# Performance work log

Measured on AMD Instinct MI355X. Metric: run time of the kernel, lower is better.

Reference implementation:

```python
import jax, jax.numpy as jnp
import numpy as np

WS = (4, 4, 4)          # window size (D, H, W)
DIM = 96
HEADS = 8
HEAD_DIM = DIM // HEADS
SCALE = HEAD_DIM ** (-0.5)
N = WS[0] * WS[1] * WS[2]  # 64 tokens per window


def _relative_position_index(ws):
    coords = np.stack(np.meshgrid(np.arange(ws[0]), np.arange(ws[1]), np.arange(ws[2]), indexing='ij'))
    cf = coords.reshape(3, -1)                       # [3, N]
    rel = cf[:, :, None] - cf[:, None, :]            # [3, N, N]
    rel = rel.transpose(1, 2, 0).astype(np.int64)    # [N, N, 3]
    rel[:, :, 0] += ws[0] - 1
    rel[:, :, 1] += ws[1] - 1
    rel[:, :, 2] += ws[2] - 1
    rel[:, :, 0] *= (2 * ws[1] - 1) * (2 * ws[2] - 1)
    rel[:, :, 1] *= 2 * ws[2] - 1
    return jnp.asarray(rel.sum(-1))                  # [N, N]

REL_IDX = _relative_position_index(WS)


def setup_inputs() -> dict:
    key = jax.random.key(0)
    ks = jax.random.split(key, 6)
    B = 4096   # total windows (64 images x 64 windows)
    nW = 64
    table_size = (2 * WS[0] - 1) * (2 * WS[1] - 1) * (2 * WS[2] - 1)  # 343
    return {
        'x': jax.random.normal(ks[0], (B, N, DIM), jnp.float32),
        'mask': jax.random.normal(ks[1], (nW, N, N), jnp.float32),
        'qkv_w': jax.random.normal(ks[2], (3 * DIM, DIM), jnp.float32) * 0.02,
        'proj_w': jax.random.normal(ks[3], (DIM, DIM), jnp.float32) * 0.02,
        'proj_b': jnp.zeros((DIM,), jnp.float32),
        'bias_table': jax.random.normal(ks[4], (table_size, HEADS), jnp.float32) * 0.02,
    }


def reference(x, mask, qkv_w, proj_w, proj_b, bias_table):
    B, n, C = x.shape
    # QKV projection (torch Linear: y = x @ W.T), split into heads
    qkv = (x @ qkv_w.T).reshape(B, n, 3, HEADS, HEAD_DIM)
    qkv = jnp.transpose(qkv, (2, 0, 3, 1, 4))        # [3, B, H, N, hd]
    q, k, v = qkv[0], qkv[1], qkv[2]
    attn = jnp.einsum('bhnd,bhmd->bhnm', q, k) * SCALE
    # gathered relative position bias: [N, N, H] -> [H, N, N]
    bias = bias_table[REL_IDX[:n, :n].reshape(-1)].reshape(n, n, HEADS)
    attn = attn + jnp.transpose(bias, (2, 0, 1))[None]
    # shifted-window mask add
    nW = mask.shape[0]
    attn = attn.reshape(B // nW, nW, HEADS, n, n) + mask[None, :, None]
    attn = attn.reshape(B, HEADS, n, n)
    attn = jax.nn.softmax(attn, axis=-1)
    out = jnp.einsum('bhnm,bhmd->bnhd', attn, v).reshape(B, n, C)
    return out @ proj_w.T + proj_b
```

## Files before the change

### kernel.cpp

```cpp
#include <hip/hip_runtime.h>
#include <hip/hip_bf16.h>
#include <stdint.h>


typedef float  f32x4  __attribute__((ext_vector_type(4)));
typedef float  f32x16 __attribute__((ext_vector_type(16)));
typedef short  short8 __attribute__((ext_vector_type(8)));

#define WS_WQKV_OFF  (8388608)
#define WS_WPROJ_OFF (8388608 + 55296)
#define LOG2E 1.4426950408889634f

__device__ __forceinline__ unsigned short f2bf(float f) {
  __hip_bfloat16 h = __float2bfloat16(f);
  return *reinterpret_cast<unsigned short*>(&h);
}
__device__ __forceinline__ uint32_t pack2(float a, float b) {
  __hip_bfloat162 h = __float22bfloat162_rn(float2{a, b});
  return *reinterpret_cast<uint32_t*>(&h);
}

__global__ void prep_weights(const float* __restrict__ qkv_w,
                             const float* __restrict__ proj_w,
                             unsigned short* __restrict__ ws16) {
  int tid = blockIdx.x * 256 + threadIdx.x;
  if (tid < 27648) {
    float v = qkv_w[tid];
    if (tid < 9216) v *= (0.28867513459481288f * LOG2E);
    ws16[WS_WQKV_OFF / 2 + tid] = f2bf(v);
  } else {
    int t = tid - 27648;
    ws16[WS_WPROJ_OFF / 2 + t] = f2bf(proj_w[t]);
  }
}

__global__ void prep_biasm(const float* __restrict__ mask,
                           const float* __restrict__ bias_table,
                           float* __restrict__ biasm) {
  int tid = blockIdx.x * 256 + threadIdx.x;
  int m = tid & 63;
  int r = (tid >> 6) & 63;
  int h = (tid >> 12) & 7;
  int w = tid >> 15;
  int dr = r >> 4, hr = (r >> 2) & 3, wr = r & 3;
  int dm = m >> 4, hm = (m >> 2) & 3, wm = m & 3;
  int idx = (dr - dm + 3) * 49 + (hr - hm + 3) * 7 + (wr - wm + 3);
  biasm[tid] = (bias_table[idx * 8 + h] + mask[(w * 64 + r) * 64 + m]) * LOG2E;
}

__global__ __launch_bounds__(512, 4) void attn_main(
    const float* __restrict__ x, const float* __restrict__ proj_b,
    const unsigned short* __restrict__ ws16, const float* __restrict__ biasm,
    float* __restrict__ out) {
  __shared__ __align__(16) unsigned short xo[64][104];
  __shared__ __align__(16) unsigned short q_s[8][64][24];
  __shared__ __align__(16) unsigned short k_s[8][64][24];
  __shared__ __align__(16) unsigned short v_s[8][16][72];

  const int tid  = threadIdx.x;
  const int wv   = tid >> 6;
  const int lane = tid & 63;
  const int lo4 = lane & 15, hi4 = lane >> 4;
  const int lo5 = lane & 31, hi5 = lane >> 5;
  const int blk = blockIdx.x;
  const int wmask = blk & 63;

  const unsigned short* wqkv  = ws16 + WS_WQKV_OFF / 2;
  const unsigned short* wproj = ws16 + WS_WPROJ_OFF / 2;

  {
    int h = tid >> 6, r = tid & 63;
    *(uint2*)&q_s[h][r][12] = make_uint2(0u, 0u);
    *(uint2*)&k_s[h][r][12] = make_uint2(0u, 0u);
  }

  {
    const float4* xsrc = (const float4*)(x + (size_t)blk * (64 * 96));
    for (int i = tid; i < 1536; i += 512) {
      float4 v = xsrc[i];
      int t = i / 24, c4 = (i % 24) * 4;
      uint2 w2;
      w2.x = pack2(v.x, v.y);
      w2.y = pack2(v.z, v.w);
      *(uint2*)&xo[t][c4] = w2;
    }
  }
  __syncthreads();

  {
    const int sub = wv & 3;
    const int par = wv >> 2;
    const int trow = sub * 16 + lo4;
    f32x4 acc[9];
#pragma unroll
    for (int i = 0; i < 9; ++i) acc[i] = (f32x4){0.f, 0.f, 0.f, 0.f};
#pragma unroll
    for (int ks = 0; ks < 3; ++ks) {
      short8 bfX = *(const short8*)&xo[trow][ks * 32 + hi4 * 8];
#pragma unroll
      for (int i = 0; i < 9; ++i) {
        const int mt = 2 * i + par;
        short8 afW = *(const short8*)&wqkv[(mt * 16 + lo4) * 96 + ks * 32 + hi4 * 8];
        acc[i] = __builtin_amdgcn_mfma_f32_16x16x32_bf16(afW, bfX, acc[i], 0, 0, 0);
      }
    }
#pragma unroll
    for (int i = 0; i < 9; ++i) {
      const int mt = 2 * i + par;
      const int o0 = mt * 16 + hi4 * 4;
      if (o0 < 192) {
        const int sec = (o0 >= 96) ? 96 : 0;
        const int o = o0 - sec;
        const int head = o / 12, ch = o - head * 12;
        uint2 w2;
        w2.x = pack2(acc[i][0], acc[i][1]);
        w2.y = pack2(acc[i][2], acc[i][3]);
        if (sec == 0) *(uint2*)&q_s[head][trow][ch] = w2;
        else          *(uint2*)&k_s[head][trow][ch] = w2;
      } else {
        const int o = o0 - 192;
        const int head = o / 12, ch = o - head * 12;
#pragma unroll
        for (int j = 0; j < 4; ++j)
          v_s[head][ch + j][trow] = f2bf(acc[i][j]);
      }
    }
  }

  f32x16 c[2][2];
  {
    const float* bm = biasm + (size_t)(wmask * 8 + wv) * 4096;
#pragma unroll
    for (int ti = 0; ti < 2; ++ti)
#pragma unroll
      for (int tj = 0; tj < 2; ++tj)
#pragma unroll
        for (int q4 = 0; q4 < 4; ++q4) {
          float4 b4 = *(const float4*)&bm[(tj * 32 + lo5) * 64 + ti * 32 + 8 * q4 + 4 * hi5];
          c[ti][tj][4 * q4 + 0] = b4.x;
          c[ti][tj][4 * q4 + 1] = b4.y;
          c[ti][tj][4 * q4 + 2] = b4.z;
          c[ti][tj][4 * q4 + 3] = b4.w;
        }
  }
  __syncthreads();

  {
    const int h = wv;
#pragma unroll
    for (int ti = 0; ti < 2; ++ti) {
      short8 af = *(const short8*)&k_s[h][ti * 32 + lo5][hi5 * 8];
#pragma unroll
      for (int tj = 0; tj < 2; ++tj) {
        short8 bf = *(const short8*)&q_s[h][tj * 32 + lo5][hi5 * 8];
        c[ti][tj] = __builtin_amdgcn_mfma_f32_32x32x16_bf16(af, bf, c[ti][tj], 0, 0, 0);
      }
    }

#pragma unroll
    for (int tj = 0; tj < 2; ++tj) {
      float mx = -1e30f;
#pragma unroll
      for (int ti = 0; ti < 2; ++ti)
#pragma unroll
        for (int reg = 0; reg < 16; ++reg) mx = fmaxf(mx, c[ti][tj][reg]);
      mx = fmaxf(mx, __shfl_xor(mx, 32));
      float sum = 0.f;
#pragma unroll
      for (int ti = 0; ti < 2; ++ti)
#pragma unroll
        for (int reg = 0; reg < 16; ++reg) {
          float e = exp2f(c[ti][tj][reg] - mx);
          c[ti][tj][reg] = e;
          sum += e;
        }
      sum += __shfl_xor(sum, 32);
      float rs = 1.0f / sum;
#pragma unroll
      for (int ti = 0; ti < 2; ++ti)
#pragma unroll
        for (int reg = 0; reg < 16; ++reg) c[ti][tj][reg] *= rs;
    }

    uint32_t pkp[2][2][8];
#pragma unroll
    for (int ti = 0; ti < 2; ++ti)
#pragma unroll
      for (int tj = 0; tj < 2; ++tj)
#pragma unroll
        for (int u = 0; u < 8; ++u)
          pkp[ti][tj][u] = pack2(c[ti][tj][2 * u], c[ti][tj][2 * u + 1]);

    f32x16 oD[2];
    oD[0] = (f32x16)(0.f); oD[1] = (f32x16)(0.f);
#pragma unroll
    for (int kc = 0; kc < 4; ++kc) {
      const int ti = kc >> 1, base = 4 * (kc & 1);
      short8 av = *(const short8*)&v_s[h][lo5 & 15][kc * 16 + hi5 * 8];
#pragma unroll
      for (int tj = 0; tj < 2; ++tj) {
        uint32_t A0 = pkp[ti][tj][base + 0], A1 = pkp[ti][tj][base + 1];
        uint32_t A2 = pkp[ti][tj][base + 2], A3 = pkp[ti][tj][base + 3];
        uint32_t k0 = hi5 ? A2 : A0, k1 = hi5 ? A3 : A1;
        uint32_t s0 = (uint32_t)__shfl_xor((int)(hi5 ? A0 : A2), 32);
        uint32_t s1 = (uint32_t)__shfl_xor((int)(hi5 ? A1 : A3), 32);
        union { uint32_t u[4]; short8 s; } bfr;
        bfr.u[0] = hi5 ? s0 : k0;
        bfr.u[1] = hi5 ? s1 : k1;
        bfr.u[2] = hi5 ? k0 : s0;
        bfr.u[3] = hi5 ? k1 : s1;
        oD[tj] = __builtin_amdgcn_mfma_f32_32x32x16_bf16(av, bfr.s, oD[tj], 0, 0, 0);
      }
    }

#pragma unroll
    for (int tj = 0; tj < 2; ++tj) {
      const int q = tj * 32 + lo5;
      uint2 w2;
      w2.x = pack2(oD[tj][0], oD[tj][1]);
      w2.y = pack2(oD[tj][2], oD[tj][3]);
      *(uint2*)&xo[q][h * 12 + 4 * hi5] = w2;
      if (hi5 == 0) {
        uint2 w3;
        w3.x = pack2(oD[tj][4], oD[tj][5]);
        w3.y = pack2(oD[tj][6], oD[tj][7]);
        *(uint2*)&xo[q][h * 12 + 8] = w3;
      }
    }
  }
  __syncthreads();

  {
    const int mt = wv >> 1;
    const int nb = (wv & 1) * 3;
    f32x4 acc[3];
#pragma unroll
    for (int nt = 0; nt < 3; ++nt) acc[nt] = (f32x4){0.f, 0.f, 0.f, 0.f};
    const int arow = mt * 16 + lo4;
#pragma unroll
    for (int ks = 0; ks < 3; ++ks) {
      short8 af = *(const short8*)&xo[arow][ks * 32 + hi4 * 8];
#pragma unroll
      for (int nt = 0; nt < 3; ++nt) {
        const int ntg = nb + nt;
        short8 bf = *(const short8*)&wproj[(ntg * 16 + lo4) * 96 + ks * 32 + hi4 * 8];
        acc[nt] = __builtin_amdgcn_mfma_f32_16x16x32_bf16(af, bf, acc[nt], 0, 0, 0);
      }
    }
    float* od = out + (size_t)blk * (64 * 96);
#pragma unroll
    for (int nt = 0; nt < 3; ++nt) {
      const int ntg = nb + nt;
      float pb = proj_b[ntg * 16 + lo4];
#pragma unroll
      for (int j = 0; j < 4; ++j)
        od[(mt * 16 + hi4 * 4 + j) * 96 + ntg * 16 + lo4] = acc[nt][j] + pb;
    }
  }
}

extern "C" void kernel_launch(void* const* d_in, const int* in_sizes, int n_in,
                              void* d_out, int out_size, void* d_ws, size_t ws_size,
                              hipStream_t stream) {
  const float* x          = (const float*)d_in[0];
  const float* mask       = (const float*)d_in[1];
  const float* qkv_w      = (const float*)d_in[2];
  const float* proj_w     = (const float*)d_in[3];
  const float* proj_b     = (const float*)d_in[4];
  const float* bias_table = (const float*)d_in[5];

  float* biasm = (float*)d_ws;
  unsigned short* ws16 = (unsigned short*)d_ws;

  prep_weights<<<144, 256, 0, stream>>>(qkv_w, proj_w, ws16);
  prep_biasm<<<8192, 256, 0, stream>>>(mask, bias_table, biasm);
  attn_main<<<4096, 512, 0, stream>>>(x, proj_b, ws16, biasm, (float*)d_out);
}
```

Baseline: 180.6 us.

## Cut shared memory footprint: register-load x, shrink q/k padding, alias output on v_s

Drops the LDS staging buffer for x. Each wave now loads its own x rows straight from global memory into registers and converts them to bf16 fragments, which also removes one barrier. The q/k LDS rows shrink from 24 to 16 elements, and the attention output is written into an alias of the v_s buffer, which costs an extra barrier before it is overwritten. With LDS usage falling from about 81KB to about 51KB, more blocks can fit per CU, and launch bounds are raised from 4 to 6. The risks are register pressure or spills under the tighter bound and possible LDS bank conflicts from the smaller row stride.

```diff
diff --git a/kernel.cpp b/kernel.cpp
--- a/kernel.cpp
+++ b/kernel.cpp
@@ -48,13 +48,12 @@
   biasm[tid] = (bias_table[idx * 8 + h] + mask[(w * 64 + r) * 64 + m]) * LOG2E;
 }
 
-__global__ __launch_bounds__(512, 4) void attn_main(
+__global__ __launch_bounds__(512, 6) void attn_main(
     const float* __restrict__ x, const float* __restrict__ proj_b,
     const unsigned short* __restrict__ ws16, const float* __restrict__ biasm,
     float* __restrict__ out) {
-  __shared__ __align__(16) unsigned short xo[64][104];
-  __shared__ __align__(16) unsigned short q_s[8][64][24];
-  __shared__ __align__(16) unsigned short k_s[8][64][24];
+  __shared__ __align__(16) unsigned short q_s[8][64][16];
+  __shared__ __align__(16) unsigned short k_s[8][64][16];
   __shared__ __align__(16) unsigned short v_s[8][16][72];
 
   const int tid  = threadIdx.x;
@@ -67,6 +66,7 @@
 
   const unsigned short* wqkv  = ws16 + WS_WQKV_OFF / 2;
   const unsigned short* wproj = ws16 + WS_WPROJ_OFF / 2;
+  unsigned short (*o_s)[104] = reinterpret_cast<unsigned short(*)[104]>(&v_s[0][0][0]);
 
   {
     int h = tid >> 6, r = tid & 63;
@@ -75,33 +75,36 @@
   }
 
   {
-    const float4* xsrc = (const float4*)(x + (size_t)blk * (64 * 96));
-    for (int i = tid; i < 1536; i += 512) {
-      float4 v = xsrc[i];
-      int t = i / 24, c4 = (i % 24) * 4;
-      uint2 w2;
-      w2.x = pack2(v.x, v.y);
-      w2.y = pack2(v.z, v.w);
-      *(uint2*)&xo[t][c4] = w2;
-    }
-  }
-  __syncthreads();
-
-  {
     const int sub = wv & 3;
     const int par = wv >> 2;
     const int trow = sub * 16 + lo4;
+    const float* xrow = x + (size_t)blk * 6144 + (size_t)trow * 96;
+    float4 xa[6];
+#pragma unroll
+    for (int ks = 0; ks < 3; ++ks) {
+      xa[2 * ks]     = *(const float4*)&xrow[ks * 32 + hi4 * 8];
+      xa[2 * ks + 1] = *(const float4*)&xrow[ks * 32 + hi4 * 8 + 4];
+    }
+    short8 bfX[3];
+#pragma unroll
+    for (int ks = 0; ks < 3; ++ks) {
+      union { uint32_t u[4]; short8 s; } t;
+      t.u[0] = pack2(xa[2 * ks].x,     xa[2 * ks].y);
+      t.u[1] = pack2(xa[2 * ks].z,     xa[2 * ks].w);
+      t.u[2] = pack2(xa[2 * ks + 1].x, xa[2 * ks + 1].y);
+      t.u[3] = pack2(xa[2 * ks + 1].z, xa[2 * ks + 1].w);
+      bfX[ks] = t.s;
+    }
     f32x4 acc[9];
 #pragma unroll
     for (int i = 0; i < 9; ++i) acc[i] = (f32x4){0.f, 0.f, 0.f, 0.f};
 #pragma unroll
     for (int ks = 0; ks < 3; ++ks) {
-      short8 bfX = *(const short8*)&xo[trow][ks * 32 + hi4 * 8];
 #pragma unroll
       for (int i = 0; i < 9; ++i) {
         const int mt = 2 * i + par;
         short8 afW = *(const short8*)&wqkv[(mt * 16 + lo4) * 96 + ks * 32 + hi4 * 8];
-        acc[i] = __builtin_amdgcn_mfma_f32_16x16x32_bf16(afW, bfX, acc[i], 0, 0, 0);
+        acc[i] = __builtin_amdgcn_mfma_f32_16x16x32_bf16(afW, bfX[ks], acc[i], 0, 0, 0);
       }
     }
 #pragma unroll
@@ -145,6 +148,7 @@
   }
   __syncthreads();
 
+  f32x16 oD[2];
   {
     const int h = wv;
 #pragma unroll
@@ -191,7 +195,6 @@
         for (int u = 0; u < 8; ++u)
           pkp[ti][tj][u] = pack2(c[ti][tj][2 * u], c[ti][tj][2 * u + 1]);
 
-    f32x16 oD[2];
     oD[0] = (f32x16)(0.f); oD[1] = (f32x16)(0.f);
 #pragma unroll
     for (int kc = 0; kc < 4; ++kc) {
@@ -212,19 +215,23 @@
         oD[tj] = __builtin_amdgcn_mfma_f32_32x32x16_bf16(av, bfr.s, oD[tj], 0, 0, 0);
       }
     }
-
+  }
+  __syncthreads();
+
+  {
+    const int h = wv;
 #pragma unroll
     for (int tj = 0; tj < 2; ++tj) {
       const int q = tj * 32 + lo5;
       uint2 w2;
       w2.x = pack2(oD[tj][0], oD[tj][1]);
       w2.y = pack2(oD[tj][2], oD[tj][3]);
-      *(uint2*)&xo[q][h * 12 + 4 * hi5] = w2;
+      *(uint2*)&o_s[q][h * 12 + 4 * hi5] = w2;
       if (hi5 == 0) {
         uint2 w3;
         w3.x = pack2(oD[tj][4], oD[tj][5]);
         w3.y = pack2(oD[tj][6], oD[tj][7]);
-        *(uint2*)&xo[q][h * 12 + 8] = w3;
+        *(uint2*)&o_s[q][h * 12 + 8] = w3;
       }
     }
   }
@@ -239,7 +246,7 @@
     const int arow = mt * 16 + lo4;
 #pragma unroll
     for (int ks = 0; ks < 3; ++ks) {
-      short8 af = *(const short8*)&xo[arow][ks * 32 + hi4 * 8];
+      short8 af = *(const short8*)&o_s[arow][ks * 32 + hi4 * 8];
 #pragma unroll
       for (int nt = 0; nt < 3; ++nt) {
         const int ntg = nb + nt;
```

Measured after the change: 190.4 us. +5.4%, slower.
